# Optimization experiments

Hardware: AMD Instinct MI355X
Metric: run time of the kernel (lower is better)

## Reference

```python
import jax, jax.numpy as jnp
import numpy as np

N_NODES = 50000
N_EDGES = 800000
IN_FEAT = 100
OUT_FEAT = 100
NUM_RELS = 200
NUM_HEADS = 3
NUM_BASES = 100
SUB_IN = 1   # in_feat // num_bases
SUB_OUT = 1  # out_feat // num_bases


def setup_inputs() -> dict:
    key = jax.random.key(0)
    ks = jax.random.split(key, 10)
    return {
        "h": jax.random.normal(ks[0], (N_NODES, IN_FEAT), jnp.float32),
        "e": jax.random.normal(ks[1], (N_EDGES, IN_FEAT), jnp.float32),
        "norm": jax.random.uniform(ks[2], (N_NODES, 1), jnp.float32),
        "weight": jax.random.normal(ks[3], (NUM_RELS, NUM_BASES * SUB_IN * SUB_OUT), jnp.float32) * 0.1,
        "attn": jax.random.normal(ks[4], (NUM_RELS, NUM_HEADS, OUT_FEAT), jnp.float32) * 0.1,
        "fc_w": jax.random.normal(ks[5], (IN_FEAT, OUT_FEAT * NUM_HEADS), jnp.float32) * 0.1,
        "loop_w": jax.random.normal(ks[6], (IN_FEAT, OUT_FEAT), jnp.float32) * 0.1,
        "rel": jax.random.randint(ks[7], (N_EDGES,), 0, NUM_RELS, jnp.int32),
        "src": jax.random.randint(ks[8], (N_EDGES,), 0, N_NODES, jnp.int32),
        "dst": jax.random.randint(ks[9], (N_EDGES,), 0, N_NODES, jnp.int32),
    }


def reference(h, e, norm, weight, attn, fc_w, loop_w, rel, src, dst):
    E = rel.shape[0]
    # --- relation-indexed block-diagonal message (torch.bmm over blocks) ---
    W_e = weight[rel].reshape(E, NUM_BASES, SUB_IN, SUB_OUT)        # per-edge block weights
    h_src = h[src].reshape(E, NUM_BASES, SUB_IN)                    # gathered src features
    msg = jnp.einsum('ebi,ebio->ebo', h_src, W_e).reshape(E, OUT_FEAT)
    # --- edge-feature attention fuse ---
    a_e = attn[rel]                                                 # (E, H, OUT)
    fc_e = (e @ fc_w).reshape(E, NUM_HEADS, OUT_FEAT)               # fc(edge)
    feat = jax.nn.leaky_relu(a_e * fc_e, 0.2).sum(axis=1)           # (E, OUT)
    msg = msg + feat
    # --- scatter-sum aggregation to dst nodes, then norm + self-loop ---
    agg = jax.ops.segment_sum(msg, dst, num_segments=N_NODES)       # (N, OUT)
    node = agg * norm
    loop_message = h @ loop_w
    return node + loop_message
```

## Files before the change

kernel.cpp:

```cpp
#include <hip/hip_runtime.h>
#include <hip/hip_bf16.h>

#define N_NODES 50000
#define N_EDGES 800000
#define IN_FEAT 100
#define OUT_FEAT 100
#define NUM_RELS 200
#define NUM_HEADS 3

#define KP 128
#define NPH 112
#define NP  336
#define MB  128
#define NT_O 7
#define WPB 8
#define SLP 116
#define MSGW 100

#define WS_B       0u
#define WS_LW      86016u
#define WS_CNT     114688u
#define WS_OFFS    315392u
#define WS_CURSOR  516096u
#define WS_BSUM    716800u
#define WS_SLOT    717056u
#define WS_PERM    3917056u
#define WS_MSG     7117056u
#define WS_NEEDED  167117056u
#define NNODES_PAD 50176

typedef __attribute__((ext_vector_type(8))) short short8;
typedef __attribute__((ext_vector_type(4))) float f32x4;

__device__ __forceinline__ unsigned short f2bf(float f) {
    unsigned u = __builtin_bit_cast(unsigned, f);
    unsigned r = u + 0x7FFFu + ((u >> 16) & 1u);
    return (unsigned short)(r >> 16);
}
__device__ __forceinline__ float bf2f(unsigned hs) {
    return __builtin_bit_cast(float, hs << 16);
}

__global__ __launch_bounds__(256) void build_B(const float* __restrict__ fc_w,
                                               unsigned short* __restrict__ Bws) {
    int idx = blockIdx.x * 256 + threadIdx.x;
    if (idx >= NP * 16) return;
    int n = idx >> 4, g = idx & 15;
    int head = n / NPH, nl = n - head * NPH;
    int kt = g >> 2, g4 = g & 3;
    unsigned p[4];
#pragma unroll
    for (int half = 0; half < 2; ++half) {
#pragma unroll
        for (int jp = 0; jp < 2; ++jp) {
            int k_lo = kt * 32 + half * 16 + g4 * 4 + jp * 2;
            int k_hi = k_lo + 1;
            float vlo = (k_lo < IN_FEAT && nl < OUT_FEAT)
                      ? fc_w[k_lo * (OUT_FEAT * NUM_HEADS) + head * OUT_FEAT + nl] : 0.f;
            float vhi = (k_hi < IN_FEAT && nl < OUT_FEAT)
                      ? fc_w[k_hi * (OUT_FEAT * NUM_HEADS) + head * OUT_FEAT + nl] : 0.f;
            p[half * 2 + jp] = (unsigned)f2bf(vlo) | ((unsigned)f2bf(vhi) << 16);
        }
    }
    unsigned off = (unsigned)(head * (NPH * KP * 2)) +
                   (((unsigned)(nl * (KP * 2) + g * 16)) ^ (((unsigned)(nl & 7)) << 4));
    *reinterpret_cast<int4*>(reinterpret_cast<char*>(Bws) + off) =
        make_int4((int)p[0], (int)p[1], (int)p[2], (int)p[3]);
}

__global__ __launch_bounds__(256) void build_LW(const float* __restrict__ loop_w,
                                                unsigned short* __restrict__ LWws) {
    int idx = blockIdx.x * 256 + threadIdx.x;
    if (idx >= NPH * 16) return;
    int nl = idx >> 4, g = idx & 15;
    int kt = g >> 2, g4 = g & 3;
    unsigned p[4];
#pragma unroll
    for (int half = 0; half < 2; ++half) {
#pragma unroll
        for (int jp = 0; jp < 2; ++jp) {
            int k_lo = kt * 32 + half * 16 + g4 * 4 + jp * 2;
            int k_hi = k_lo + 1;
            float vlo = (k_lo < IN_FEAT && nl < OUT_FEAT) ? loop_w[k_lo * OUT_FEAT + nl] : 0.f;
            float vhi = (k_hi < IN_FEAT && nl < OUT_FEAT) ? loop_w[k_hi * OUT_FEAT + nl] : 0.f;
            p[half * 2 + jp] = (unsigned)f2bf(vlo) | ((unsigned)f2bf(vhi) << 16);
        }
    }
    reinterpret_cast<int4*>(LWws)[idx] = make_int4((int)p[0], (int)p[1], (int)p[2], (int)p[3]);
}

__global__ __launch_bounds__(512, 2) void loop_gemm(const float* __restrict__ h,
                                                    const unsigned short* __restrict__ LWimg,
                                                    float* __restrict__ out) {
    const int tid = threadIdx.x;
    const int wave = tid >> 6, lane = tid & 63;
    const int lrow = lane & 15, lk = lane >> 4;
    const int rbase = blockIdx.x * MB;
    const int grow = rbase + wave * 16 + lrow;
    const bool ok = grow < N_NODES;
    const float* ap = h + (size_t)grow * IN_FEAT;

    short8 afrag[4];
#pragma unroll
    for (int kt = 0; kt < 4; ++kt) {
        int k0 = kt * 32 + lk * 4, k1 = k0 + 16;
        float4 va = (ok && k0 + 4 <= IN_FEAT) ? *reinterpret_cast<const float4*>(ap + k0)
                                              : make_float4(0.f, 0.f, 0.f, 0.f);
        float4 vb = (ok && k1 + 4 <= IN_FEAT) ? *reinterpret_cast<const float4*>(ap + k1)
                                              : make_float4(0.f, 0.f, 0.f, 0.f);
        afrag[kt][0] = (short)f2bf(va.x); afrag[kt][1] = (short)f2bf(va.y);
        afrag[kt][2] = (short)f2bf(va.z); afrag[kt][3] = (short)f2bf(va.w);
        afrag[kt][4] = (short)f2bf(vb.x); afrag[kt][5] = (short)f2bf(vb.y);
        afrag[kt][6] = (short)f2bf(vb.z); afrag[kt][7] = (short)f2bf(vb.w);
    }

#pragma unroll
    for (int nt = 0; nt < NT_O; ++nt) {
        f32x4 acc = (f32x4){0.f, 0.f, 0.f, 0.f};
#pragma unroll
        for (int kt = 0; kt < 4; ++kt) {
            short8 bfrag = *reinterpret_cast<const short8*>(
                LWimg + ((nt * 16 + lrow) * KP + kt * 32 + lk * 8));
            acc = __builtin_amdgcn_mfma_f32_16x16x32_bf16(afrag[kt], bfrag, acc, 0, 0, 0);
        }
        int o = nt * 16 + lrow;
        if (o < OUT_FEAT) {
#pragma unroll
            for (int r = 0; r < 4; ++r) {
                int crow = rbase + wave * 16 + lk * 4 + r;
                if (crow < N_NODES) out[(size_t)crow * OUT_FEAT + o] = acc[r];
            }
        }
    }
}

__global__ __launch_bounds__(512) void hist_kernel(const int* __restrict__ dst,
                                                   int* __restrict__ cnt) {
    int e = blockIdx.x * 512 + threadIdx.x;
    if (e < N_EDGES) atomicAdd(&cnt[dst[e]], 1);
}

__global__ __launch_bounds__(1024) void scan1(const int* __restrict__ cnt,
                                              int* __restrict__ offs,
                                              int* __restrict__ bsum) {
    __shared__ int s[1024];
    int i = blockIdx.x * 1024 + threadIdx.x;
    int v = (i < N_NODES) ? cnt[i] : 0;
    s[threadIdx.x] = v;
    __syncthreads();
    for (int d = 1; d < 1024; d <<= 1) {
        int t = (threadIdx.x >= d) ? s[threadIdx.x - d] : 0;
        __syncthreads();
        s[threadIdx.x] += t;
        __syncthreads();
    }
    offs[i] = s[threadIdx.x] - v;
    if (threadIdx.x == 1023) bsum[blockIdx.x] = s[1023];
}

__global__ __launch_bounds__(64) void scan2(int* __restrict__ bsum) {
    __shared__ int s[64];
    int v = (threadIdx.x < NNODES_PAD / 1024) ? bsum[threadIdx.x] : 0;
    s[threadIdx.x] = v;
    __syncthreads();
    for (int d = 1; d < 64; d <<= 1) {
        int t = (threadIdx.x >= d) ? s[threadIdx.x - d] : 0;
        __syncthreads();
        s[threadIdx.x] += t;
        __syncthreads();
    }
    bsum[threadIdx.x] = s[threadIdx.x] - v;
}

__global__ __launch_bounds__(1024) void scan3(int* __restrict__ offs,
                                              const int* __restrict__ bsum,
                                              int* __restrict__ cursor) {
    int i = blockIdx.x * 1024 + threadIdx.x;
    int v = offs[i] + bsum[blockIdx.x];
    offs[i] = v;
    cursor[i] = v;
}

__global__ __launch_bounds__(512) void scatter_kernel(const int* __restrict__ dst,
                                                      int* __restrict__ cursor,
                                                      int* __restrict__ perm,
                                                      int* __restrict__ slotmap) {
    int e = blockIdx.x * 512 + threadIdx.x;
    if (e < N_EDGES) {
        int p = atomicAdd(&cursor[dst[e]], 1);
        perm[p] = e;
        slotmap[e] = p;
    }
}

template<bool TOWS>
__global__ __launch_bounds__(512, 2) void feat_kernel(
        const float* __restrict__ efeat, const int* __restrict__ rel,
        const unsigned short* __restrict__ Bimg, const float* __restrict__ attn,
        const float* __restrict__ h, const float* __restrict__ weight,
        const float* __restrict__ norm, const int* __restrict__ src,
        const int* __restrict__ dst, const int* __restrict__ slotmap,
        float* __restrict__ out, unsigned short* __restrict__ msgws,
        int ntiles) {

    __shared__ __align__(16) unsigned short Blds[NP * KP];
    __shared__ __align__(16) unsigned short slice[WPB][16 * SLP];

    const int tid = threadIdx.x;
    {
        const int4* sp = reinterpret_cast<const int4*>(Bimg);
        int4* dp = reinterpret_cast<int4*>(Blds);
        for (int i = tid; i < NP * KP / 8; i += 512) dp[i] = sp[i];
    }
    __syncthreads();

    const int wave = tid >> 6, lane = tid & 63;
    const int lrow = lane & 15, lk = lane >> 4;
    const int gstride = gridDim.x * WPB;
    int tile = blockIdx.x * WPB + wave;
    if (tile >= ntiles) return;

    const char* Bc = reinterpret_cast<const char*>(Blds);
    int bkt[4];
#pragma unroll
    for (int kt = 0; kt < 4; ++kt)
        bkt[kt] = lrow * (KP * 2) + ((kt * 64 + lk * 16) ^ ((lrow & 7) << 4));

    float4 pa[8];
    int prl[4];
    {
        const float* ap = efeat + (size_t)(tile * 16 + lrow) * IN_FEAT;
#pragma unroll
        for (int kt = 0; kt < 4; ++kt) {
            int k0 = kt * 32 + lk * 4, k1 = k0 + 16;
            pa[kt * 2]     = (k0 + 4 <= IN_FEAT) ? *reinterpret_cast<const float4*>(ap + k0)
                                                 : make_float4(0.f, 0.f, 0.f, 0.f);
            pa[kt * 2 + 1] = (k1 + 4 <= IN_FEAT) ? *reinterpret_cast<const float4*>(ap + k1)
                                                 : make_float4(0.f, 0.f, 0.f, 0.f);
        }
        const int* rp = rel + tile * 16 + lk * 4;
#pragma unroll
        for (int r = 0; r < 4; ++r) prl[r] = rp[r];
    }

    while (true) {
        const int cur = tile;
        const int tb = cur * 16;
        short8 afrag[4];
#pragma unroll
        for (int kt = 0; kt < 4; ++kt) {
            float4 va = pa[kt * 2], vb = pa[kt * 2 + 1];
            afrag[kt][0] = (short)f2bf(va.x); afrag[kt][1] = (short)f2bf(va.y);
            afrag[kt][2] = (short)f2bf(va.z); afrag[kt][3] = (short)f2bf(va.w);
            afrag[kt][4] = (short)f2bf(vb.x); afrag[kt][5] = (short)f2bf(vb.y);
            afrag[kt][6] = (short)f2bf(vb.z); afrag[kt][7] = (short)f2bf(vb.w);
        }
        int aoff[4];
#pragma unroll
        for (int r = 0; r < 4; ++r) aoff[r] = prl[r] * (NUM_HEADS * OUT_FEAT);

        int next = tile + gstride;
        bool more = next < ntiles;
        {
            int pidx = more ? next : cur;
            const float* ap = efeat + (size_t)(pidx * 16 + lrow) * IN_FEAT;
#pragma unroll
            for (int kt = 0; kt < 4; ++kt) {
                int k0 = kt * 32 + lk * 4, k1 = k0 + 16;
                pa[kt * 2]     = (k0 + 4 <= IN_FEAT) ? *reinterpret_cast<const float4*>(ap + k0)
                                                     : make_float4(0.f, 0.f, 0.f, 0.f);
                pa[kt * 2 + 1] = (k1 + 4 <= IN_FEAT) ? *reinterpret_cast<const float4*>(ap + k1)
                                                     : make_float4(0.f, 0.f, 0.f, 0.f);
            }
            const int* rp = rel + pidx * 16 + lk * 4;
#pragma unroll
            for (int r = 0; r < 4; ++r) prl[r] = rp[r];
        }

        float feat[NT_O][4];
#pragma unroll
        for (int nt = 0; nt < NT_O; ++nt)
#pragma unroll
            for (int r = 0; r < 4; ++r) feat[nt][r] = 0.f;

#pragma unroll 1
        for (int hh = 0; hh < NUM_HEADS; ++hh) {
            const char* Bh = Bc + hh * (NPH * KP * 2);
#pragma unroll
            for (int nt = 0; nt < NT_O; ++nt) {
                f32x4 acc = (f32x4){0.f, 0.f, 0.f, 0.f};
#pragma unroll
                for (int kt = 0; kt < 4; ++kt) {
                    short8 bfrag = *reinterpret_cast<const short8*>(
                        Bh + bkt[kt] + nt * 4096);
                    acc = __builtin_amdgcn_mfma_f32_16x16x32_bf16(afrag[kt], bfrag, acc, 0, 0, 0);
                }
                int o = nt * 16 + lrow;
                if (o < OUT_FEAT) {
                    int oo = hh * OUT_FEAT + o;
#pragma unroll
                    for (int r = 0; r < 4; ++r) {
                        float v = acc[r] * attn[aoff[r] + oo];
                        feat[nt][r] += (v > 0.f) ? v : 0.2f * v;
                    }
                }
            }
        }

        if (TOWS) {
            unsigned short* sl = slice[wave];
#pragma unroll
            for (int nt = 0; nt < NT_O; ++nt) {
                int o = nt * 16 + lrow;
                if (o < OUT_FEAT) {
#pragma unroll
                    for (int r = 0; r < 4; ++r)
                        sl[(lk * 4 + r) * SLP + o] = f2bf(feat[nt][r]);
                }
            }
            asm volatile("s_waitcnt lgkmcnt(0)" ::: "memory");
            __builtin_amdgcn_sched_barrier(0);
            const int row = lane >> 2, part = lane & 3;
            const int slot = slotmap[tb + row];
            const unsigned long long* sq =
                reinterpret_cast<const unsigned long long*>(slice[wave]);
            unsigned long long* mq = reinterpret_cast<unsigned long long*>(msgws);
#pragma unroll
            for (int j = 0; j < 7; ++j) {
                int idx = part + 4 * j;
                if (idx < 25)
                    mq[(size_t)slot * 25 + idx] = sq[row * (SLP / 4) + idx];
            }
        } else {
            int sr_r[4], d_r[4]; float nm_r[4]; int rl_r[4];
#pragma unroll
            for (int r = 0; r < 4; ++r) {
                int ei = tb + lk * 4 + r;
                sr_r[r] = src[ei]; d_r[r] = dst[ei]; nm_r[r] = norm[d_r[r]];
                rl_r[r] = aoff[r] / (NUM_HEADS * OUT_FEAT);
            }
#pragma unroll
            for (int nt = 0; nt < NT_O; ++nt) {
                int o = nt * 16 + lrow;
                if (o < OUT_FEAT) {
#pragma unroll
                    for (int r = 0; r < 4; ++r) {
                        float mg = h[(size_t)sr_r[r] * IN_FEAT + o] *
                                   weight[(size_t)rl_r[r] * OUT_FEAT + o];
                        atomicAdd(&out[(size_t)d_r[r] * OUT_FEAT + o],
                                  (mg + feat[nt][r]) * nm_r[r]);
                    }
                }
            }
        }

        if (!more) break;
        tile = next;
    }
}

__global__ __launch_bounds__(256, 2) void agg_kernel(
        const unsigned short* __restrict__ msgws, const int* __restrict__ offs,
        const int* __restrict__ cnt, const int* __restrict__ perm,
        const int* __restrict__ src, const int* __restrict__ rel,
        const float* __restrict__ h, const float* __restrict__ weight,
        const float* __restrict__ norm, float* __restrict__ out) {
    int wv = threadIdx.x >> 6, lane = threadIdx.x & 63;
    int n = blockIdx.x * 4 + wv;
    if (n >= N_NODES) return;
    int start = offs[n], deg = cnt[n];
    if (deg == 0 || lane >= OUT_FEAT / 2) return;
    const unsigned* mp = reinterpret_cast<const unsigned*>(msgws);
    float ax = 0.f, ay = 0.f;
    int k = start, end = start + deg;
    for (; k + 2 <= end; k += 2) {
        int e0 = perm[k], e1 = perm[k + 1];
        int s0 = src[e0], s1 = src[e1];
        int r0 = rel[e0], r1 = rel[e1];
        unsigned u0 = mp[(size_t)k * (MSGW / 2) + lane];
        unsigned u1 = mp[(size_t)(k + 1) * (MSGW / 2) + lane];
        float2 h0 = *reinterpret_cast<const float2*>(h + (size_t)s0 * IN_FEAT + 2 * lane);
        float2 w0 = *reinterpret_cast<const float2*>(weight + (size_t)r0 * OUT_FEAT + 2 * lane);
        float2 h1 = *reinterpret_cast<const float2*>(h + (size_t)s1 * IN_FEAT + 2 * lane);
        float2 w1 = *reinterpret_cast<const float2*>(weight + (size_t)r1 * OUT_FEAT + 2 * lane);
        ax += h0.x * w0.x + bf2f(u0 & 0xffffu) + h1.x * w1.x + bf2f(u1 & 0xffffu);
        ay += h0.y * w0.y + bf2f(u0 >> 16) + h1.y * w1.y + bf2f(u1 >> 16);
    }
    if (k < end) {
        int e0 = perm[k];
        int s0 = src[e0], r0 = rel[e0];
        unsigned u0 = mp[(size_t)k * (MSGW / 2) + lane];
        float2 h0 = *reinterpret_cast<const float2*>(h + (size_t)s0 * IN_FEAT + 2 * lane);
        float2 w0 = *reinterpret_cast<const float2*>(weight + (size_t)r0 * OUT_FEAT + 2 * lane);
        ax += h0.x * w0.x + bf2f(u0 & 0xffffu);
        ay += h0.y * w0.y + bf2f(u0 >> 16);
    }
    float nm = norm[n];
    float2* op = reinterpret_cast<float2*>(out + (size_t)n * OUT_FEAT) + lane;
    float2 curv = *op;
    curv.x += ax * nm; curv.y += ay * nm;
    *op = curv;
}

extern "C" void kernel_launch(void* const* d_in, const int* in_sizes, int n_in,
                              void* d_out, int out_size, void* d_ws, size_t ws_size,
                              hipStream_t stream) {
    const float* h      = (const float*)d_in[0];
    const float* efeat  = (const float*)d_in[1];
    const float* norm   = (const float*)d_in[2];
    const float* weight = (const float*)d_in[3];
    const float* attn   = (const float*)d_in[4];
    const float* fc_w   = (const float*)d_in[5];
    const float* loop_w = (const float*)d_in[6];
    const int*   rel    = (const int*)d_in[7];
    const int*   src    = (const int*)d_in[8];
    const int*   dst    = (const int*)d_in[9];
    float* out = (float*)d_out;

    char* ws = (char*)d_ws;
    unsigned short* Bimg  = (unsigned short*)(ws + WS_B);
    unsigned short* LWimg = (unsigned short*)(ws + WS_LW);
    int* cnt     = (int*)(ws + WS_CNT);
    int* offs    = (int*)(ws + WS_OFFS);
    int* cursor  = (int*)(ws + WS_CURSOR);
    int* bsum    = (int*)(ws + WS_BSUM);
    int* slotmap = (int*)(ws + WS_SLOT);
    int* perm    = (int*)(ws + WS_PERM);
    unsigned short* msgws = (unsigned short*)(ws + WS_MSG);

    build_B<<<(NP * 16 + 255) / 256, 256, 0, stream>>>(fc_w, Bimg);
    build_LW<<<(NPH * 16 + 255) / 256, 256, 0, stream>>>(loop_w, LWimg);
    loop_gemm<<<(N_NODES + MB - 1) / MB, 512, 0, stream>>>(h, LWimg, out);

    const int ntiles = N_EDGES / 16;

    if (ws_size >= (size_t)WS_NEEDED) {
        hipMemsetAsync(cnt, 0, NNODES_PAD * sizeof(int), stream);
        hist_kernel<<<(N_EDGES + 511) / 512, 512, 0, stream>>>(dst, cnt);
        scan1<<<NNODES_PAD / 1024, 1024, 0, stream>>>(cnt, offs, bsum);
        scan2<<<1, 64, 0, stream>>>(bsum);
        scan3<<<NNODES_PAD / 1024, 1024, 0, stream>>>(offs, bsum, cursor);
        scatter_kernel<<<(N_EDGES + 511) / 512, 512, 0, stream>>>(dst, cursor, perm, slotmap);

        feat_kernel<true><<<256, 512, 0, stream>>>(
            efeat, rel, Bimg, attn, h, weight, norm, src, dst, slotmap,
            out, msgws, ntiles);
        agg_kernel<<<(N_NODES + 3) / 4, 256, 0, stream>>>(
            msgws, offs, cnt, perm, src, rel, h, weight, norm, out);
    } else {
        feat_kernel<false><<<256, 512, 0, stream>>>(
            efeat, rel, Bimg, attn, h, weight, norm, src, dst, nullptr,
            out, msgws, ntiles);
    }
}
```

Measured before the change: 440.2 us.

## Pack src/rel into sorted meta, shrink LDS, drop slice staging, double grid

The scatter kernel now writes a packed (src | rel<<16) word per sorted slot instead of a permutation index, so the aggregation kernel no longer does two dependent gathers per edge. The fc weight image in LDS is compacted from 336 to 312 rows and the per-wave staging slice is removed, with bf16 features written straight to the message workspace via the per-row slot map. The smaller LDS footprint is meant to let more blocks fit per CU, so the feat grid is doubled and the agg kernel's launch bounds are raised. The trade-off is scattered 2-byte global stores instead of coalesced 8-byte ones, and the packing assumes src < 65536.

```diff
diff --git a/kernel.cpp b/kernel.cpp
--- a/kernel.cpp
+++ b/kernel.cpp
@@ -10,12 +10,12 @@
 
 #define KP 128
 #define NPH 112
-#define NP  336
 #define MB  128
 #define NT_O 7
 #define WPB 8
-#define SLP 116
 #define MSGW 100
+#define BROWS 312
+#define HSTRIDE 25600
 
 #define WS_B       0u
 #define WS_LW      86016u
@@ -24,7 +24,7 @@
 #define WS_CURSOR  516096u
 #define WS_BSUM    716800u
 #define WS_SLOT    717056u
-#define WS_PERM    3917056u
+#define WS_META    3917056u
 #define WS_MSG     7117056u
 #define WS_NEEDED  167117056u
 #define NNODES_PAD 50176
@@ -44,26 +44,27 @@
 __global__ __launch_bounds__(256) void build_B(const float* __restrict__ fc_w,
                                                unsigned short* __restrict__ Bws) {
     int idx = blockIdx.x * 256 + threadIdx.x;
-    if (idx >= NP * 16) return;
+    if (idx >= BROWS * 16) return;
     int n = idx >> 4, g = idx & 15;
-    int head = n / NPH, nl = n - head * NPH;
+    int head = n / 100, nl = n - head * 100;
     int kt = g >> 2, g4 = g & 3;
-    unsigned p[4];
-#pragma unroll
-    for (int half = 0; half < 2; ++half) {
-#pragma unroll
-        for (int jp = 0; jp < 2; ++jp) {
-            int k_lo = kt * 32 + half * 16 + g4 * 4 + jp * 2;
-            int k_hi = k_lo + 1;
-            float vlo = (k_lo < IN_FEAT && nl < OUT_FEAT)
-                      ? fc_w[k_lo * (OUT_FEAT * NUM_HEADS) + head * OUT_FEAT + nl] : 0.f;
-            float vhi = (k_hi < IN_FEAT && nl < OUT_FEAT)
-                      ? fc_w[k_hi * (OUT_FEAT * NUM_HEADS) + head * OUT_FEAT + nl] : 0.f;
-            p[half * 2 + jp] = (unsigned)f2bf(vlo) | ((unsigned)f2bf(vhi) << 16);
-        }
-    }
-    unsigned off = (unsigned)(head * (NPH * KP * 2)) +
-                   (((unsigned)(nl * (KP * 2) + g * 16)) ^ (((unsigned)(nl & 7)) << 4));
+    unsigned p[4] = {0u, 0u, 0u, 0u};
+    if (n < 300) {
+#pragma unroll
+        for (int half = 0; half < 2; ++half) {
+#pragma unroll
+            for (int jp = 0; jp < 2; ++jp) {
+                int k_lo = kt * 32 + half * 16 + g4 * 4 + jp * 2;
+                int k_hi = k_lo + 1;
+                float vlo = (k_lo < IN_FEAT)
+                          ? fc_w[k_lo * (OUT_FEAT * NUM_HEADS) + head * OUT_FEAT + nl] : 0.f;
+                float vhi = (k_hi < IN_FEAT)
+                          ? fc_w[k_hi * (OUT_FEAT * NUM_HEADS) + head * OUT_FEAT + nl] : 0.f;
+                p[half * 2 + jp] = (unsigned)f2bf(vlo) | ((unsigned)f2bf(vhi) << 16);
+            }
+        }
+    }
+    unsigned off = (unsigned)(n * 256) + (((unsigned)(g * 16)) ^ (((unsigned)(nl & 7)) << 4));
     *reinterpret_cast<int4*>(reinterpret_cast<char*>(Bws) + off) =
         make_int4((int)p[0], (int)p[1], (int)p[2], (int)p[3]);
 }
@@ -182,14 +183,16 @@
 }
 
 __global__ __launch_bounds__(512) void scatter_kernel(const int* __restrict__ dst,
+                                                      const int* __restrict__ src,
+                                                      const int* __restrict__ rel,
                                                       int* __restrict__ cursor,
-                                                      int* __restrict__ perm,
-                                                      int* __restrict__ slotmap) {
+                                                      int* __restrict__ slotmap,
+                                                      int* __restrict__ meta) {
     int e = blockIdx.x * 512 + threadIdx.x;
     if (e < N_EDGES) {
         int p = atomicAdd(&cursor[dst[e]], 1);
-        perm[p] = e;
         slotmap[e] = p;
+        meta[p] = (src[e] & 0xFFFF) | (rel[e] << 16);
     }
 }
 
@@ -203,14 +206,13 @@
         float* __restrict__ out, unsigned short* __restrict__ msgws,
         int ntiles) {
 
-    __shared__ __align__(16) unsigned short Blds[NP * KP];
-    __shared__ __align__(16) unsigned short slice[WPB][16 * SLP];
+    __shared__ __align__(16) unsigned short Blds[BROWS * 128];
 
     const int tid = threadIdx.x;
     {
         const int4* sp = reinterpret_cast<const int4*>(Bimg);
         int4* dp = reinterpret_cast<int4*>(Blds);
-        for (int i = tid; i < NP * KP / 8; i += 512) dp[i] = sp[i];
+        for (int i = tid; i < BROWS * 128 / 8; i += 512) dp[i] = sp[i];
     }
     __syncthreads();
 
@@ -224,7 +226,7 @@
     int bkt[4];
 #pragma unroll
     for (int kt = 0; kt < 4; ++kt)
-        bkt[kt] = lrow * (KP * 2) + ((kt * 64 + lk * 16) ^ ((lrow & 7) << 4));
+        bkt[kt] = lrow * 256 + ((kt * 64 + lk * 16) ^ ((lrow & 7) << 4));
 
     float4 pa[8];
     int prl[4];
@@ -259,6 +261,12 @@
 #pragma unroll
         for (int r = 0; r < 4; ++r) aoff[r] = prl[r] * (NUM_HEADS * OUT_FEAT);
 
+        int slot_r[4];
+        if (TOWS) {
+#pragma unroll
+            for (int r = 0; r < 4; ++r) slot_r[r] = slotmap[tb + lk * 4 + r];
+        }
+
         int next = tile + gstride;
         bool more = next < ntiles;
         {
@@ -285,7 +293,7 @@
 
 #pragma unroll 1
         for (int hh = 0; hh < NUM_HEADS; ++hh) {
-            const char* Bh = Bc + hh * (NPH * KP * 2);
+            const char* Bh = Bc + hh * HSTRIDE;
 #pragma unroll
             for (int nt = 0; nt < NT_O; ++nt) {
                 f32x4 acc = (f32x4){0.f, 0.f, 0.f, 0.f};
@@ -308,28 +316,14 @@
         }
 
         if (TOWS) {
-            unsigned short* sl = slice[wave];
 #pragma unroll
             for (int nt = 0; nt < NT_O; ++nt) {
                 int o = nt * 16 + lrow;
                 if (o < OUT_FEAT) {
 #pragma unroll
                     for (int r = 0; r < 4; ++r)
-                        sl[(lk * 4 + r) * SLP + o] = f2bf(feat[nt][r]);
+                        msgws[(size_t)slot_r[r] * MSGW + o] = f2bf(feat[nt][r]);
                 }
-            }
-            asm volatile("s_waitcnt lgkmcnt(0)" ::: "memory");
-            __builtin_amdgcn_sched_barrier(0);
-            const int row = lane >> 2, part = lane & 3;
-            const int slot = slotmap[tb + row];
-            const unsigned long long* sq =
-                reinterpret_cast<const unsigned long long*>(slice[wave]);
-            unsigned long long* mq = reinterpret_cast<unsigned long long*>(msgws);
-#pragma unroll
-            for (int j = 0; j < 7; ++j) {
-                int idx = part + 4 * j;
-                if (idx < 25)
-                    mq[(size_t)slot * 25 + idx] = sq[row * (SLP / 4) + idx];
             }
         } else {
             int sr_r[4], d_r[4]; float nm_r[4]; int rl_r[4];
@@ -359,10 +353,9 @@
     }
 }
 
-__global__ __launch_bounds__(256, 2) void agg_kernel(
+__global__ __launch_bounds__(256, 4) void agg_kernel(
         const unsigned short* __restrict__ msgws, const int* __restrict__ offs,
-        const int* __restrict__ cnt, const int* __restrict__ perm,
-        const int* __restrict__ src, const int* __restrict__ rel,
+        const int* __restrict__ cnt, const int* __restrict__ meta,
         const float* __restrict__ h, const float* __restrict__ weight,
         const float* __restrict__ norm, float* __restrict__ out) {
     int wv = threadIdx.x >> 6, lane = threadIdx.x & 63;
@@ -374,9 +367,9 @@
     float ax = 0.f, ay = 0.f;
     int k = start, end = start + deg;
     for (; k + 2 <= end; k += 2) {
-        int e0 = perm[k], e1 = perm[k + 1];
-        int s0 = src[e0], s1 = src[e1];
-        int r0 = rel[e0], r1 = rel[e1];
+        int m0 = meta[k], m1 = meta[k + 1];
+        int s0 = m0 & 0xFFFF, s1 = m1 & 0xFFFF;
+        int r0 = (unsigned)m0 >> 16, r1 = (unsigned)m1 >> 16;
         unsigned u0 = mp[(size_t)k * (MSGW / 2) + lane];
         unsigned u1 = mp[(size_t)(k + 1) * (MSGW / 2) + lane];
         float2 h0 = *reinterpret_cast<const float2*>(h + (size_t)s0 * IN_FEAT + 2 * lane);
@@ -387,8 +380,8 @@
         ay += h0.y * w0.y + bf2f(u0 >> 16) + h1.y * w1.y + bf2f(u1 >> 16);
     }
     if (k < end) {
-        int e0 = perm[k];
-        int s0 = src[e0], r0 = rel[e0];
+        int m0 = meta[k];
+        int s0 = m0 & 0xFFFF, r0 = (unsigned)m0 >> 16;
         unsigned u0 = mp[(size_t)k * (MSGW / 2) + lane];
         float2 h0 = *reinterpret_cast<const float2*>(h + (size_t)s0 * IN_FEAT + 2 * lane);
         float2 w0 = *reinterpret_cast<const float2*>(weight + (size_t)r0 * OUT_FEAT + 2 * lane);
@@ -425,10 +418,10 @@
     int* cursor  = (int*)(ws + WS_CURSOR);
     int* bsum    = (int*)(ws + WS_BSUM);
     int* slotmap = (int*)(ws + WS_SLOT);
-    int* perm    = (int*)(ws + WS_PERM);
+    int* meta    = (int*)(ws + WS_META);
     unsigned short* msgws = (unsigned short*)(ws + WS_MSG);
 
-    build_B<<<(NP * 16 + 255) / 256, 256, 0, stream>>>(fc_w, Bimg);
+    build_B<<<(BROWS * 16 + 255) / 256, 256, 0, stream>>>(fc_w, Bimg);
     build_LW<<<(NPH * 16 + 255) / 256, 256, 0, stream>>>(loop_w, LWimg);
     loop_gemm<<<(N_NODES + MB - 1) / MB, 512, 0, stream>>>(h, LWimg, out);
 
@@ -440,15 +433,16 @@
         scan1<<<NNODES_PAD / 1024, 1024, 0, stream>>>(cnt, offs, bsum);
         scan2<<<1, 64, 0, stream>>>(bsum);
         scan3<<<NNODES_PAD / 1024, 1024, 0, stream>>>(offs, bsum, cursor);
-        scatter_kernel<<<(N_EDGES + 511) / 512, 512, 0, stream>>>(dst, cursor, perm, slotmap);
-
-        feat_kernel<true><<<256, 512, 0, stream>>>(
+        scatter_kernel<<<(N_EDGES + 511) / 512, 512, 0, stream>>>(
+            dst, src, rel, cursor, slotmap, meta);
+
+        feat_kernel<true><<<512, 512, 0, stream>>>(
             efeat, rel, Bimg, attn, h, weight, norm, src, dst, slotmap,
             out, msgws, ntiles);
         agg_kernel<<<(N_NODES + 3) / 4, 256, 0, stream>>>(
-            msgws, offs, cnt, perm, src, rel, h, weight, norm, out);
+            msgws, offs, cnt, meta, h, weight, norm, out);
     } else {
-        feat_kernel<false><<<256, 512, 0, stream>>>(
+        feat_kernel<false><<<512, 512, 0, stream>>>(
             efeat, rel, Bimg, attn, h, weight, norm, src, dst, nullptr,
             out, msgws, ntiles);
     }
```

After: 407.4 us. 1.08x faster.
